# Optimization experiments

Measured on AMD Instinct MI355X. Metric: run time of the kernel, lower is better.

## Reference

```python
import jax, jax.numpy as jnp
import numpy as np

K = 10  # beam width / topk from init


def topk_compo_seq(compo_logits, k=K):
    # log-softmax scores, then step-wise beam-search merge (top_k of k*k combos)
    scores = jax.nn.log_softmax(compo_logits, axis=-1)  # [B, S, V]
    B, S, V = scores.shape

    def step(carry, x):
        seq_scores, topk_seq = carry  # [B,k], [B,k,S]
        step_scores, i = x            # [B,V], scalar step index
        curr_scores, curr_idx = jax.lax.top_k(step_scores, k)          # [B,k]
        comb = (seq_scores[:, :, None] + curr_scores[:, None, :]).reshape(B, k * k)
        new_scores, top_idx = jax.lax.top_k(comb, k)                   # [B,k]
        r = top_idx // k   # which previous beam
        c = top_idx % k    # which current candidate
        prev = jnp.take_along_axis(topk_seq, r[:, :, None], axis=1)    # [B,k,S]
        tok = jnp.take_along_axis(curr_idx, c, axis=1).astype(jnp.int32)  # [B,k]
        new_seq = jax.lax.dynamic_update_slice(prev, tok[:, :, None], (0, 0, i))
        return (new_scores, new_seq), None

    init = (jnp.zeros((B, k), scores.dtype), jnp.zeros((B, k, S), jnp.int32))
    xs = (jnp.swapaxes(scores, 0, 1), jnp.arange(S))
    (seq_scores, topk_seq), _ = jax.lax.scan(step, init, xs)
    return topk_seq, seq_scores


def setup_inputs() -> dict:
    key = jax.random.key(0)
    k1, k2, k3, k4 = jax.random.split(key, 4)
    B, S, V_SC, V_COMPO = 512, 40, 7000, 1000
    return {
        "pred_char_struc": jax.random.randint(k1, (B,), 0, 3, dtype=jnp.int32),
        "pred_sc_logits": jax.random.normal(k2, (B, V_SC), jnp.float32),
        "pred_lr_compo_logits": jax.random.normal(k3, (B, S, V_COMPO), jnp.float32),
        "pred_ul_compo_logits": jax.random.normal(k4, (B, S, V_COMPO), jnp.float32),
    }


def reference(pred_char_struc, pred_sc_logits, pred_lr_compo_logits, pred_ul_compo_logits):
    _, pred_sc_labels = jax.lax.top_k(pred_sc_logits, K)          # [B,K]
    pred_lr_compo_seq, _ = topk_compo_seq(pred_lr_compo_logits)   # [B,K,S]
    pred_ul_compo_seq, _ = topk_compo_seq(pred_ul_compo_logits)   # [B,K,S]

    B, _, S = pred_lr_compo_seq.shape
    # stage != 'train': assemble per-sample results. The TF scatter/scatter_add
    # into a zero tensor with disjoint batch indices is exactly a per-batch select.
    sc_full = jnp.zeros((B, K, S), jnp.int32).at[:, :, 0].set(pred_sc_labels.astype(jnp.int32))
    struc = pred_char_struc[:, None, None]
    pred_results = jnp.where(struc == 0, sc_full,
                   jnp.where(struc == 1, pred_lr_compo_seq,
                   jnp.where(struc == 2, pred_ul_compo_seq, 0)))
    return pred_sc_labels, pred_lr_compo_seq, pred_ul_compo_seq, pred_results
```

## Files before the change

kernel.cpp:

```cpp
#include <hip/hip_runtime.h>
#include <math.h>

#define PB   512
#define PS   40
#define VSC  7000
#define VC   1000
#define PK   10
#define BK   (PB * PK)
#define BKS  (PB * PK * PS)

__device__ __forceinline__ unsigned int ord_u32(float f) {
    unsigned int u = __float_as_uint(f);
    return (u & 0x80000000u) ? ~u : (u | 0x80000000u);
}
__device__ __forceinline__ float inv_ord(unsigned int ou) {
    return __uint_as_float((ou & 0x80000000u) ? (ou & 0x7fffffffu) : ~ou);
}

__device__ __forceinline__ void load_row16(const float* __restrict__ row, int lane, float* x) {
    const float4* r4 = (const float4*)row;
#pragma unroll
    for (int j = 0; j < 4; ++j) {
        int fi = (j << 6) + lane;
        float4 v;
        if (fi < VC / 4) v = r4[fi];
        else v = make_float4(-INFINITY, -INFINITY, -INFINITY, -INFINITY);
        x[j * 4 + 0] = v.x; x[j * 4 + 1] = v.y; x[j * 4 + 2] = v.z; x[j * 4 + 3] = v.w;
    }
}

__device__ __forceinline__ void wave_argmax(const float* x, int lane, float& xmax, int& amax) {
    float bv = -INFINITY; int bi = 0;
#pragma unroll
    for (int m = 0; m < 16; ++m) { if (x[m] > bv) { bv = x[m]; bi = m; } }
    int gidx = ((bi >> 2) << 8) + (lane << 2) + (bi & 3);
    unsigned long long key =
        ((unsigned long long)ord_u32(bv) << 32) |
        (unsigned long long)(0xFFFFFFFFu - (unsigned int)gidx);
#pragma unroll
    for (int off = 1; off < 64; off <<= 1) {
        unsigned long long o = __shfl_xor(key, off, 64);
        if (o > key) key = o;
    }
    xmax = inv_ord((unsigned int)(key >> 32));
    amax = (int)(0xFFFFFFFFu - (unsigned int)(key & 0xFFFFFFFFu));
}

__device__ __forceinline__ float wave_sumexp(const float* x, float xmax) {
    float s = 0.0f;
#pragma unroll
    for (int m = 0; m < 16; ++m) s += expf(x[m] - xmax);
#pragma unroll
    for (int off = 1; off < 64; off <<= 1) s += __shfl_xor(s, off, 64);
    return s;
}

__global__ __launch_bounds__(256) void topk_sc_kernel(const float* __restrict__ sc,
                                                      int* __restrict__ out) {
    const int b = blockIdx.x;
    const int t = threadIdx.x;
    const float* row = sc + (size_t)b * VSC;

    float v[28];
#pragma unroll
    for (int i = 0; i < 28; ++i) {
        int idx = t + (i << 8);
        v[i] = (idx < VSC) ? row[idx] : -INFINITY;
    }

    __shared__ unsigned long long wk[4];
    __shared__ int winner;

    for (int r = 0; r < PK; ++r) {
        float bv = -INFINITY; int bi = 0;
#pragma unroll
        for (int i = 0; i < 28; ++i) { if (v[i] > bv) { bv = v[i]; bi = i; } }
        int gidx = t + (bi << 8);
        unsigned long long key =
            ((unsigned long long)ord_u32(bv) << 32) |
            (unsigned long long)(0xFFFFFFFFu - (unsigned int)gidx);
#pragma unroll
        for (int off = 1; off < 64; off <<= 1) {
            unsigned long long o = __shfl_xor(key, off, 64);
            if (o > key) key = o;
        }
        if ((t & 63) == 0) wk[t >> 6] = key;
        __syncthreads();
        if (t == 0) {
            unsigned long long k0 = wk[0];
            if (wk[1] > k0) k0 = wk[1];
            if (wk[2] > k0) k0 = wk[2];
            if (wk[3] > k0) k0 = wk[3];
            int widx = (int)(0xFFFFFFFFu - (unsigned int)(k0 & 0xFFFFFFFFu));
            winner = widx;
            out[b * PK + r] = widx;
        }
        __syncthreads();
        int w = winner;
        if ((w & 255) == t) v[w >> 8] = -INFINITY;
    }
}

__global__ __launch_bounds__(256) void argmax_compo_kernel(const float* __restrict__ lr,
                                                           const float* __restrict__ ul,
                                                           int* __restrict__ out,
                                                           int* __restrict__ tflag) {
    const int row  = blockIdx.x * 4 + (threadIdx.x >> 6);
    const int lane = threadIdx.x & 63;
    const int tensor = (row >= PB * PS) ? 1 : 0;
    const int r2 = row - tensor * (PB * PS);
    const float* src = (tensor ? ul : lr) + (size_t)r2 * VC;

    float x[16];
    load_row16(src, lane, x);
    float xmax; int amax;
    wave_argmax(x, lane, xmax, amax);

    float se = wave_sumexp(x, xmax);
    float L = logf(se);
    float negL = 0.0f - L;
    int tcnt = 0;
#pragma unroll
    for (int m = 0; m < 16; ++m) {
        float scv = (x[m] - xmax) - L;
        tcnt += (scv == negL) ? 1 : 0;
    }
#pragma unroll
    for (int off = 1; off < 64; off <<= 1) tcnt += __shfl_xor(tcnt, off, 64);

    if (lane == 0) {
        int b = r2 / PS, s = r2 - (r2 / PS) * PS;
        out[BK + (size_t)tensor * BKS + (size_t)b * (PK * PS) + s] = amax;
        if (tcnt > 1) tflag[tensor * PB + b] = 1;
    }
}

__global__ __launch_bounds__(256) void assemble_kernel(const int* __restrict__ struc,
                                                       int* __restrict__ out) {
    const int tid = blockIdx.x * 256 + threadIdx.x;
    if (tid >= BKS) return;
    const int b   = tid / (PK * PS);
    const int rem = tid - b * (PK * PS);
    const int j   = rem / PS;
    const int s   = rem - j * PS;

    int* lrslab = out + BK;
    int* ulslab = out + BK + BKS;
    const int lrv = lrslab[b * (PK * PS) + s];
    const int ulv = ulslab[b * (PK * PS) + s];

    if (j != 0) { lrslab[tid] = lrv; ulslab[tid] = ulv; }

    const int st = struc[b];
    int res = 0;
    if (st == 1)      res = lrv;
    else if (st == 2) res = ulv;
    else if (st == 0) res = (s == 0) ? out[b * PK + j] : 0;
    out[BK + 2 * BKS + tid] = res;
}

__global__ __launch_bounds__(64) void fix_ties_kernel(const float* __restrict__ lr,
                                                      const float* __restrict__ ul,
                                                      const int* __restrict__ struc,
                                                      const int* __restrict__ tflag,
                                                      int* __restrict__ out) {
    const int id = blockIdx.x;
    if (tflag[id] == 0) return;
    const int tensor = (id >= PB) ? 1 : 0;
    const int b = id - tensor * PB;
    const int lane = threadIdx.x;
    const float* src = (tensor ? ul : lr) + (size_t)b * PS * VC;

    __shared__ int seq[PK][PS];
    __shared__ int tokpos[PK];
    __shared__ int t_sh;

    for (int i = 0; i < PS; ++i) {
        float x[16];
        load_row16(src + (size_t)i * VC, lane, x);
        float xmax; int amax;
        wave_argmax(x, lane, xmax, amax);
        float se = wave_sumexp(x, xmax);
        float L = logf(se);
        float negL = 0.0f - L;

        int rank_base = 0;
        unsigned long long below = (lane == 0) ? 0ull : ((~0ull) >> (64 - lane));
#pragma unroll
        for (int j = 0; j < 4; ++j) {
            int bit[4];
            unsigned long long Be[4];
#pragma unroll
            for (int e = 0; e < 4; ++e) {
                float scv = (x[j * 4 + e] - xmax) - L;
                bit[e] = (scv == negL) ? 1 : 0;
                Be[e] = __ballot(bit[e]);
            }
            int pre_lane = 0;
#pragma unroll
            for (int e = 0; e < 4; ++e) pre_lane += __popcll(Be[e] & below);
            int within = 0;
#pragma unroll
            for (int e = 0; e < 4; ++e) {
                if (bit[e]) {
                    int rk = rank_base + pre_lane + within;
                    if (rk < PK) tokpos[rk] = (j << 8) + (lane << 2) + e;
                    ++within;
                }
            }
            int grp = 0;
#pragma unroll
            for (int e = 0; e < 4; ++e) grp += __popcll(Be[e]);
            rank_base += grp;
        }
        if (lane == 0) t_sh = (rank_base < PK) ? rank_base : PK;
        __syncthreads();
        const int t = t_sh;

        int newrow[PS];
        if (lane < PK) {
            const int rsrc = lane / t;
#pragma unroll
            for (int q = 0; q < PS; ++q) newrow[q] = seq[rsrc][q];
        }
        __syncthreads();
        if (lane < PK) {
#pragma unroll
            for (int q = 0; q < PS; ++q) seq[lane][q] = newrow[q];
            seq[lane][i] = tokpos[lane % t];
        }
        __syncthreads();
    }

    int* slab = out + BK + (size_t)tensor * BKS + (size_t)b * (PK * PS);
    for (int q = lane; q < PK * PS; q += 64) slab[q] = seq[q / PS][q % PS];
    if (struc[b] == tensor + 1) {
        int* res = out + BK + 2 * BKS + (size_t)b * (PK * PS);
        for (int q = lane; q < PK * PS; q += 64) res[q] = seq[q / PS][q % PS];
    }
}

extern "C" void kernel_launch(void* const* d_in, const int* in_sizes, int n_in,
                              void* d_out, int out_size, void* d_ws, size_t ws_size,
                              hipStream_t stream) {
    const int*   struc = (const int*)d_in[0];
    const float* sc    = (const float*)d_in[1];
    const float* lr    = (const float*)d_in[2];
    const float* ul    = (const float*)d_in[3];
    int* out   = (int*)d_out;
    int* tflag = (int*)d_ws;

    hipMemsetAsync(d_ws, 0, 2 * PB * sizeof(int), stream);
    hipLaunchKernelGGL(topk_sc_kernel, dim3(PB), dim3(256), 0, stream, sc, out);
    hipLaunchKernelGGL(argmax_compo_kernel, dim3((2 * PB * PS) / 4), dim3(256), 0, stream,
                       lr, ul, out, tflag);
    hipLaunchKernelGGL(assemble_kernel, dim3((BKS + 255) / 256), dim3(256), 0, stream,
                       struc, out);
    hipLaunchKernelGGL(fix_ties_kernel, dim3(2 * PB), dim3(64), 0, stream,
                       lr, ul, struc, tflag, out);
}
```

Measured before the change: 307.8 us.

## Replace tie-fix pass with per-row rank table and closed-form beam reconstruction

The per-row pass now records, for every row, how many positions tie at the maximum log-softmax score and the first ten of those positions, written to a small workspace. A new build kernel rebuilds each beam's sequence by mixed-radix decoding of the beam index backwards over steps, one thread per (batch, beam). This removes the memset, the serial 40-step tie-fixing kernel (which reloaded every row of flagged batches) and the separate assemble pass. The trade-off is the ballot/popcount ranking on every row and a serial per-thread loop with dependent divisions in the build kernel.

```diff
diff --git a/kernel.cpp b/kernel.cpp
--- a/kernel.cpp
+++ b/kernel.cpp
@@ -8,13 +8,11 @@
 #define PK   10
 #define BK   (PB * PK)
 #define BKS  (PB * PK * PS)
+#define NROW (2 * PB * PS)
 
 __device__ __forceinline__ unsigned int ord_u32(float f) {
     unsigned int u = __float_as_uint(f);
     return (u & 0x80000000u) ? ~u : (u | 0x80000000u);
-}
-__device__ __forceinline__ float inv_ord(unsigned int ou) {
-    return __uint_as_float((ou & 0x80000000u) ? (ou & 0x7fffffffu) : ~ou);
 }
 
 __device__ __forceinline__ void load_row16(const float* __restrict__ row, int lane, float* x) {
@@ -29,21 +27,13 @@
     }
 }
 
-__device__ __forceinline__ void wave_argmax(const float* x, int lane, float& xmax, int& amax) {
-    float bv = -INFINITY; int bi = 0;
+__device__ __forceinline__ float wave_max(const float* x) {
+    float bv = -INFINITY;
 #pragma unroll
-    for (int m = 0; m < 16; ++m) { if (x[m] > bv) { bv = x[m]; bi = m; } }
-    int gidx = ((bi >> 2) << 8) + (lane << 2) + (bi & 3);
-    unsigned long long key =
-        ((unsigned long long)ord_u32(bv) << 32) |
-        (unsigned long long)(0xFFFFFFFFu - (unsigned int)gidx);
+    for (int m = 0; m < 16; ++m) bv = fmaxf(bv, x[m]);
 #pragma unroll
-    for (int off = 1; off < 64; off <<= 1) {
-        unsigned long long o = __shfl_xor(key, off, 64);
-        if (o > key) key = o;
-    }
-    xmax = inv_ord((unsigned int)(key >> 32));
-    amax = (int)(0xFFFFFFFFu - (unsigned int)(key & 0xFFFFFFFFu));
+    for (int off = 1; off < 64; off <<= 1) bv = fmaxf(bv, __shfl_xor(bv, off, 64));
+    return bv;
 }
 
 __device__ __forceinline__ float wave_sumexp(const float* x, float xmax) {
@@ -101,10 +91,10 @@
     }
 }
 
-__global__ __launch_bounds__(256) void argmax_compo_kernel(const float* __restrict__ lr,
-                                                           const float* __restrict__ ul,
-                                                           int* __restrict__ out,
-                                                           int* __restrict__ tflag) {
+__global__ __launch_bounds__(256) void rowrank_kernel(const float* __restrict__ lr,
+                                                      const float* __restrict__ ul,
+                                                      unsigned short* __restrict__ ws_t,
+                                                      unsigned short* __restrict__ ws_pos) {
     const int row  = blockIdx.x * 4 + (threadIdx.x >> 6);
     const int lane = threadIdx.x & 63;
     const int tensor = (row >= PB * PS) ? 1 : 0;
@@ -113,130 +103,78 @@
 
     float x[16];
     load_row16(src, lane, x);
-    float xmax; int amax;
-    wave_argmax(x, lane, xmax, amax);
+    const float xmax = wave_max(x);
+    const float se = wave_sumexp(x, xmax);
+    const float L = logf(se);
+    const float negL = 0.0f - L;
 
-    float se = wave_sumexp(x, xmax);
-    float L = logf(se);
-    float negL = 0.0f - L;
-    int tcnt = 0;
+    int rank_base = 0;
+    unsigned long long below = (lane == 0) ? 0ull : ((~0ull) >> (64 - lane));
 #pragma unroll
-    for (int m = 0; m < 16; ++m) {
-        float scv = (x[m] - xmax) - L;
-        tcnt += (scv == negL) ? 1 : 0;
+    for (int j = 0; j < 4; ++j) {
+        int bit[4];
+        unsigned long long Be[4];
+#pragma unroll
+        for (int e = 0; e < 4; ++e) {
+            float scv = (x[j * 4 + e] - xmax) - L;
+            bit[e] = (scv == negL) ? 1 : 0;
+            Be[e] = __ballot(bit[e]);
+        }
+        int pre_lane = 0;
+#pragma unroll
+        for (int e = 0; e < 4; ++e) pre_lane += __popcll(Be[e] & below);
+        int within = 0;
+#pragma unroll
+        for (int e = 0; e < 4; ++e) {
+            if (bit[e]) {
+                int rk = rank_base + pre_lane + within;
+                if (rk < PK) ws_pos[row * PK + rk] =
+                    (unsigned short)((j << 8) + (lane << 2) + e);
+                ++within;
+            }
+        }
+        int grp = 0;
+#pragma unroll
+        for (int e = 0; e < 4; ++e) grp += __popcll(Be[e]);
+        rank_base += grp;
     }
-#pragma unroll
-    for (int off = 1; off < 64; off <<= 1) tcnt += __shfl_xor(tcnt, off, 64);
-
-    if (lane == 0) {
-        int b = r2 / PS, s = r2 - (r2 / PS) * PS;
-        out[BK + (size_t)tensor * BKS + (size_t)b * (PK * PS) + s] = amax;
-        if (tcnt > 1) tflag[tensor * PB + b] = 1;
-    }
+    if (lane == 0) ws_t[row] = (unsigned short)((rank_base < PK) ? rank_base : PK);
 }
 
-__global__ __launch_bounds__(256) void assemble_kernel(const int* __restrict__ struc,
-                                                       int* __restrict__ out) {
+__global__ __launch_bounds__(256) void build_kernel(const int* __restrict__ struc,
+                                                    const unsigned short* __restrict__ ws_t,
+                                                    const unsigned short* __restrict__ ws_pos,
+                                                    int* __restrict__ out) {
     const int tid = blockIdx.x * 256 + threadIdx.x;
-    if (tid >= BKS) return;
-    const int b   = tid / (PK * PS);
-    const int rem = tid - b * (PK * PS);
-    const int j   = rem / PS;
-    const int s   = rem - j * PS;
+    if (tid >= PB * PK) return;
+    const int b = tid / PK;
+    const int j = tid - b * PK;
 
-    int* lrslab = out + BK;
-    int* ulslab = out + BK + BKS;
-    const int lrv = lrslab[b * (PK * PS) + s];
-    const int ulv = ulslab[b * (PK * PS) + s];
+    int* lrslab = out + BK + (size_t)b * (PK * PS) + (size_t)j * PS;
+    int* ulslab = out + BK + BKS + (size_t)b * (PK * PS) + (size_t)j * PS;
+    int* res    = out + BK + 2 * BKS + (size_t)b * (PK * PS) + (size_t)j * PS;
+    const int st = struc[b];
 
-    if (j != 0) { lrslab[tid] = lrv; ulslab[tid] = ulv; }
-
-    const int st = struc[b];
-    int res = 0;
-    if (st == 1)      res = lrv;
-    else if (st == 2) res = ulv;
-    else if (st == 0) res = (s == 0) ? out[b * PK + j] : 0;
-    out[BK + 2 * BKS + tid] = res;
-}
-
-__global__ __launch_bounds__(64) void fix_ties_kernel(const float* __restrict__ lr,
-                                                      const float* __restrict__ ul,
-                                                      const int* __restrict__ struc,
-                                                      const int* __restrict__ tflag,
-                                                      int* __restrict__ out) {
-    const int id = blockIdx.x;
-    if (tflag[id] == 0) return;
-    const int tensor = (id >= PB) ? 1 : 0;
-    const int b = id - tensor * PB;
-    const int lane = threadIdx.x;
-    const float* src = (tensor ? ul : lr) + (size_t)b * PS * VC;
-
-    __shared__ int seq[PK][PS];
-    __shared__ int tokpos[PK];
-    __shared__ int t_sh;
-
-    for (int i = 0; i < PS; ++i) {
-        float x[16];
-        load_row16(src + (size_t)i * VC, lane, x);
-        float xmax; int amax;
-        wave_argmax(x, lane, xmax, amax);
-        float se = wave_sumexp(x, xmax);
-        float L = logf(se);
-        float negL = 0.0f - L;
-
-        int rank_base = 0;
-        unsigned long long below = (lane == 0) ? 0ull : ((~0ull) >> (64 - lane));
 #pragma unroll
-        for (int j = 0; j < 4; ++j) {
-            int bit[4];
-            unsigned long long Be[4];
-#pragma unroll
-            for (int e = 0; e < 4; ++e) {
-                float scv = (x[j * 4 + e] - xmax) - L;
-                bit[e] = (scv == negL) ? 1 : 0;
-                Be[e] = __ballot(bit[e]);
-            }
-            int pre_lane = 0;
-#pragma unroll
-            for (int e = 0; e < 4; ++e) pre_lane += __popcll(Be[e] & below);
-            int within = 0;
-#pragma unroll
-            for (int e = 0; e < 4; ++e) {
-                if (bit[e]) {
-                    int rk = rank_base + pre_lane + within;
-                    if (rk < PK) tokpos[rk] = (j << 8) + (lane << 2) + e;
-                    ++within;
-                }
-            }
-            int grp = 0;
-#pragma unroll
-            for (int e = 0; e < 4; ++e) grp += __popcll(Be[e]);
-            rank_base += grp;
+    for (int tensor = 0; tensor < 2; ++tensor) {
+        int* slab = tensor ? ulslab : lrslab;
+        const int rbase = tensor * (PB * PS) + b * PS;
+        int jc = j;
+        for (int i = PS - 1; i >= 0; --i) {
+            const int t = (int)ws_t[rbase + i];
+            const int q = jc / t;
+            const int c = jc - q * t;
+            const int tok = (int)ws_pos[(rbase + i) * PK + c];
+            slab[i] = tok;
+            if (st == tensor + 1) res[i] = tok;
+            jc = q;
         }
-        if (lane == 0) t_sh = (rank_base < PK) ? rank_base : PK;
-        __syncthreads();
-        const int t = t_sh;
-
-        int newrow[PS];
-        if (lane < PK) {
-            const int rsrc = lane / t;
-#pragma unroll
-            for (int q = 0; q < PS; ++q) newrow[q] = seq[rsrc][q];
-        }
-        __syncthreads();
-        if (lane < PK) {
-#pragma unroll
-            for (int q = 0; q < PS; ++q) seq[lane][q] = newrow[q];
-            seq[lane][i] = tokpos[lane % t];
-        }
-        __syncthreads();
     }
-
-    int* slab = out + BK + (size_t)tensor * BKS + (size_t)b * (PK * PS);
-    for (int q = lane; q < PK * PS; q += 64) slab[q] = seq[q / PS][q % PS];
-    if (struc[b] == tensor + 1) {
-        int* res = out + BK + 2 * BKS + (size_t)b * (PK * PS);
-        for (int q = lane; q < PK * PS; q += 64) res[q] = seq[q / PS][q % PS];
+    if (st == 0) {
+        const int scv = out[b * PK + j];
+        for (int i = 0; i < PS; ++i) res[i] = (i == 0) ? scv : 0;
+    } else if (st != 1 && st != 2) {
+        for (int i = 0; i < PS; ++i) res[i] = 0;
     }
 }
 
@@ -247,15 +185,14 @@
     const float* sc    = (const float*)d_in[1];
     const float* lr    = (const float*)d_in[2];
     const float* ul    = (const float*)d_in[3];
-    int* out   = (int*)d_out;
-    int* tflag = (int*)d_ws;
+    int* out = (int*)d_out;
 
-    hipMemsetAsync(d_ws, 0, 2 * PB * sizeof(int), stream);
+    unsigned short* ws_t   = (unsigned short*)d_ws;
+    unsigned short* ws_pos = ws_t + NROW;
+
     hipLaunchKernelGGL(topk_sc_kernel, dim3(PB), dim3(256), 0, stream, sc, out);
-    hipLaunchKernelGGL(argmax_compo_kernel, dim3((2 * PB * PS) / 4), dim3(256), 0, stream,
-                       lr, ul, out, tflag);
-    hipLaunchKernelGGL(assemble_kernel, dim3((BKS + 255) / 256), dim3(256), 0, stream,
-                       struc, out);
-    hipLaunchKernelGGL(fix_ties_kernel, dim3(2 * PB), dim3(64), 0, stream,
-                       lr, ul, struc, tflag, out);
+    hipLaunchKernelGGL(rowrank_kernel, dim3(NROW / 4), dim3(256), 0, stream,
+                       lr, ul, ws_t, ws_pos);
+    hipLaunchKernelGGL(build_kernel, dim3((PB * PK + 255) / 256), dim3(256), 0, stream,
+                       struc, ws_t, ws_pos, out);
 }
```

Result: faster. 251.4 us (-18.3%).
